# Kernel optimization log

Hardware: AMD Instinct MI355X
Metric: run time of the kernel (lower is better)

Reference implementation:

```python
import jax, jax.numpy as jnp
import numpy as np
import math

MID = 48       # mid_channels
HEADS = 4      # num_heads
POS = 16       # mid_channels // 3 (row/col positional channels)


def _unfold(x, p):
    """nn.Unfold with kernel p, padding p//2: (..., H, W) -> (..., p, p, H, W)."""
    H, W = x.shape[-2], x.shape[-1]
    pad = p // 2
    xp = jnp.pad(x, [(0, 0)] * (x.ndim - 2) + [(pad, pad), (pad, pad)])
    return jnp.stack(
        [jnp.stack([xp[..., k:k + H, l:l + W] for l in range(p)], axis=-3)
         for k in range(p)], axis=-4)


def _pe_mlp(idx, w1, b1, g, b, w2, b2):
    """Conv2d(1->16,1x1) -> LayerNorm(16) -> Swish -> Conv2d(16->POS,1x1) on scalar coords."""
    t = idx.reshape(-1, 1)                         # (N,1)
    h = t @ w1.T + b1                              # (N,16)
    mu = jnp.mean(h, -1, keepdims=True)
    var = jnp.var(h, -1, keepdims=True)
    h = (h - mu) * jax.lax.rsqrt(var + 1e-5) * g + b
    h = h * jax.nn.sigmoid(h)                      # Swish
    e = h @ w2.T + b2                              # (N,POS)
    return e.reshape(idx.shape + (e.shape[-1],))   # (V,P,P,POS)


def setup_inputs() -> dict:
    key = jax.random.key(0)
    ks = jax.random.split(key, 32)
    B, Cin, G, H, W, P, Cout = 2, 32, 4, 28, 28, 7, 64

    def n(k, shp, s=0.05):
        return jax.random.normal(k, shp, dtype=jnp.float32) * s

    inp = {"x": jax.random.normal(ks[0], (B, Cin, G, H, W), dtype=jnp.float32)}
    inp["Wq"] = n(ks[1], (MID * HEADS, Cin)); inp["bq"] = n(ks[2], (MID * HEADS,))
    inp["Wk"] = n(ks[3], (MID * HEADS, Cin)); inp["bk"] = n(ks[4], (MID * HEADS,))
    inp["Wv"] = n(ks[5], (MID * HEADS, Cin)); inp["bv"] = n(ks[6], (MID * HEADS,))
    inp["Wout"] = n(ks[7], (Cout, MID * HEADS)); inp["bout"] = n(ks[8], (Cout,))
    inp["row_w1"] = n(ks[9], (16, 1)); inp["row_b1"] = n(ks[10], (16,))
    inp["row_ln_g"] = jnp.ones((16,), jnp.float32); inp["row_ln_b"] = jnp.zeros((16,), jnp.float32)
    inp["row_w2"] = n(ks[11], (POS, 16)); inp["row_b2"] = n(ks[12], (POS,))
    inp["col_w1"] = n(ks[13], (16, 1)); inp["col_b1"] = n(ks[14], (16,))
    inp["col_ln_g"] = jnp.ones((16,), jnp.float32); inp["col_ln_b"] = jnp.zeros((16,), jnp.float32)
    inp["col_w2"] = n(ks[15], (POS, 16)); inp["col_b2"] = n(ks[16], (POS,))
    inp["group_emb"] = n(ks[17], (G, MID - 2 * POS))
    # rotated relative spatial positions, normalized to [-1, 1]
    lin = np.linspace(-1.0, 1.0, P).astype(np.float32)
    r = np.repeat(lin[:, None], P, 1)
    c = np.repeat(lin[None, :], P, 0)
    rows, cols = [], []
    for v in range(G):
        th = v * math.pi / 2.0
        rows.append(math.cos(th) * r - math.sin(th) * c)
        cols.append(math.sin(th) * r + math.cos(th) * c)
    inp["row_indices"] = jnp.asarray(np.stack(rows, 0))
    inp["col_indices"] = jnp.asarray(np.stack(cols, 0))
    # acted relative group positions for cyclic group C4
    ar = np.arange(G)
    gi = (ar[:, None, None] + ar[None, None, :] - ar[None, :, None]) % G
    inp["g_indices"] = jnp.asarray(gi, dtype=jnp.int32)
    return inp


def _forward(x, Wq, bq, Wk, bk, Wv, bv, Wout, bout,
             row_w1, row_b1, row_ln_g, row_ln_b, row_w2, row_b2,
             col_w1, col_b1, col_ln_g, col_ln_b, col_w2, col_b2,
             group_emb, row_indices, col_indices, g_indices):
    B, Cin, G, H, W = x.shape
    P = row_indices.shape[-1]
    sqn = jnp.sqrt(jnp.float32(Cin))

    def proj(Wm, bm):  # 1x1 Conv3d -> (B, MID, HEADS, G, H, W)
        y = jnp.einsum('oi,bigyx->bogyx', Wm, x) + bm[None, :, None, None, None]
        return y.reshape(B, MID, HEADS, G, H, W)

    q = proj(Wq, bq)
    k = proj(Wk, bk)
    v = proj(Wv, bv)
    k_loc = _unfold(k, P)   # (B, MID, HEADS, G, P, P, H, W)
    v_loc = _unfold(v, P)

    content = jnp.einsum('bchgij,bchmklij->bhgijmkl', q, k_loc)
    row_e = _pe_mlp(row_indices, row_w1, row_b1, row_ln_g, row_ln_b, row_w2, row_b2)
    col_e = _pe_mlp(col_indices, col_w1, col_b1, col_ln_g, col_ln_b, col_w2, col_b2)
    row_s = jnp.einsum('bchgij,vklc->bhvgijkl', q[:, :POS], row_e)
    col_s = jnp.einsum('bchgij,vklc->bhvgijkl', q[:, POS:2 * POS], col_e)
    g_e = group_emb[g_indices]                              # (V, G, M, gdim)
    g_s = jnp.einsum('bchgij,vgmc->bhvgijm', q[:, 2 * POS:], g_e)

    # scores: (b, h, v, g, i, j, m, k, l)
    scores = (row_s[:, :, :, :, :, :, None] + col_s[:, :, :, :, :, :, None]
              + g_s[..., None, None] + content[:, :, None]) / sqn

    # mask patch positions that fall outside the image (-inf -> prob 0)
    valid = _unfold(jnp.ones((H, W), jnp.float32), P)       # (P, P, H, W)
    valid = jnp.transpose(valid, (2, 3, 0, 1))[None, None, None, None, :, :, None, :, :]
    scores = jnp.where(valid > 0.5, scores, -jnp.inf)

    shp = scores.shape
    probs = jax.nn.softmax(scores.reshape(shp[:-3] + (-1,)), axis=-1).reshape(shp)

    o = jnp.einsum('bhvgijmkl,bchmklij->bchvij', probs, v_loc)  # (B, MID, HEADS, V, H, W)
    o = o.reshape(B, MID * HEADS, G, H, W)
    return jnp.einsum('oi,bivyx->bovyx', Wout, o) + bout[None, :, None, None, None]


def reference(x, Wq, bq, Wk, bk, Wv, bv, Wout, bout,
              row_w1, row_b1, row_ln_g, row_ln_b, row_w2, row_b2,
              col_w1, col_b1, col_ln_g, col_ln_b, col_w2, col_b2,
              group_emb, row_indices, col_indices, g_indices):
    return _forward(x, Wq, bq, Wk, bk, Wv, bv, Wout, bout,
                    row_w1, row_b1, row_ln_g, row_ln_b, row_w2, row_b2,
                    col_w1, col_b1, col_ln_g, col_ln_b, col_w2, col_b2,
                    group_emb, row_indices, col_indices, g_indices)
```

## Files before the change

### kernel.cpp

```cpp
#include <hip/hip_runtime.h>
#include <math.h>

#define Bb   2
#define CIN  32
#define Gg   4
#define NH   4
#define Hh   28
#define Ww   28
#define HW   784
#define Pp   7
#define PP   49
#define MID  48
#define COUT 64
#define OC   192

#define QF    0
#define KF    602112
#define VF    1204224
#define OOFF  1806336
#define KBH   75264
#define KM    18816
#define VBH   75264
#define VPL   37632

#define KSCALE 0.2550611135387359f

__device__ unsigned g_peT2[Gg * PP * 16];
__device__ unsigned g_geT2[8 * 64];
__device__ float    g_WT2[OC * COUT];
__device__ float    g_WqT[CIN * OC];
__device__ float    g_WkT[CIN * OC];
__device__ float    g_WvT[CIN * OC];

typedef _Float16 h2f __attribute__((ext_vector_type(2)));

__device__ __forceinline__ unsigned packh2(float a, float b) {
    auto r = __builtin_amdgcn_cvt_pkrtz(a, b);
    return __builtin_bit_cast(unsigned, r);
}

__device__ __forceinline__ float fdot2(unsigned a, unsigned b, float c) {
    return __builtin_amdgcn_fdot2(__builtin_bit_cast(h2f, a),
                                  __builtin_bit_cast(h2f, b), c, false);
}

__device__ __forceinline__ float exp2_fast(float x) {
    float r;
    asm("v_exp_f32 %0, %1" : "=v"(r) : "v"(x));
    return r;
}

__global__ __launch_bounds__(256) void prep_kernel(
    const float* row_w1, const float* row_b1,
    const float* row_g,  const float* row_bb,
    const float* row_w2, const float* row_b2,
    const float* col_w1, const float* col_b1,
    const float* col_g,  const float* col_bb,
    const float* col_w2, const float* col_b2,
    const float* row_idx, const float* col_idx,
    const float* group_emb, const int* g_indices,
    const float* Wout,
    const float* __restrict__ Wq, const float* __restrict__ Wk,
    const float* __restrict__ Wv)
{
    __shared__ float wtmp[16 * 193];
    int tid = threadIdx.x;
    if (blockIdx.x == 1) {
        for (int idx = tid; idx < OC * CIN; idx += 256) {
            int oo = idx >> 5, ci = idx & 31;
            int tp = ci * OC + oo;
            g_WqT[tp] = Wq[idx];
            g_WkT[tp] = Wk[idx];
            g_WvT[tp] = Wv[idx];
        }
        return;
    }
    for (int t = tid; t < 2 * Gg * PP; t += 256) {
        int half = t / (Gg * PP);
        int n    = t - half * (Gg * PP);
        int v = n / PP, kl = n % PP;
        const float* w1 = half ? col_w1 : row_w1;
        const float* b1 = half ? col_b1 : row_b1;
        const float* lg = half ? col_g  : row_g;
        const float* lb = half ? col_bb : row_bb;
        const float* w2 = half ? col_w2 : row_w2;
        const float* b2 = half ? col_b2 : row_b2;
        float tv = half ? col_idx[n] : row_idx[n];

        float hb[16];
        float mean = 0.f;
        for (int k = 0; k < 16; k++) { hb[k] = tv * w1[k] + b1[k]; mean += hb[k]; }
        mean *= (1.f / 16.f);
        float var = 0.f;
        for (int k = 0; k < 16; k++) { float d = hb[k] - mean; var += d * d; }
        var *= (1.f / 16.f);
        float inv = 1.f / sqrtf(var + 1e-5f);
        for (int k = 0; k < 16; k++) {
            float hn = (hb[k] - mean) * inv * lg[k] + lb[k];
            hb[k] = hn / (1.f + expf(-hn));
        }
        float accv[16];
        for (int p = 0; p < 16; p++) {
            float acc = b2[p];
            for (int k = 0; k < 16; k++) acc += hb[k] * w2[p * 16 + k];
            accv[p] = acc * KSCALE;
        }
        for (int i2 = 0; i2 < 8; i2++)
            g_peT2[(v * PP + kl) * 16 + half * 8 + i2] =
                packh2(accv[2 * i2], accv[2 * i2 + 1]);
    }
    for (int t = tid; t < 64; t += 256) {
        int gi = g_indices[t];
        for (int i2 = 0; i2 < 8; i2++)
            g_geT2[i2 * 64 + t] = packh2(group_emb[gi * 16 + 2 * i2] * KSCALE,
                                         group_emb[gi * 16 + 2 * i2 + 1] * KSCALE);
    }
    for (int chunk = 0; chunk < 4; chunk++) {
        int obase = chunk * 16;
        __syncthreads();
        for (int idx = tid; idx < 16 * OC; idx += 256) {
            int ol = idx / OC, t = idx % OC;
            wtmp[ol * 193 + t] = Wout[(obase + ol) * OC + t];
        }
        __syncthreads();
        for (int idx = tid; idx < 16 * OC; idx += 256) {
            int tp = idx / 16, ol = idx % 16;
            int h = tp / MID, c = tp % MID;
            g_WT2[tp * 64 + obase + ol] = wtmp[ol * 193 + c * NH + h];
        }
    }
}

__global__ __launch_bounds__(192) void qkvpe_kernel(const float* __restrict__ x,
    const float* __restrict__ bq, const float* __restrict__ bk,
    const float* __restrict__ bv, float* __restrict__ ws)
{
    __shared__ float xs[2 * CIN * 8];
    int tid = threadIdx.x;
    unsigned* uw = (unsigned*)ws;

    int r = blockIdx.x;
    int jq = r & 3; r >>= 2;
    int i = r % Hh; r /= Hh;
    int gp = r & 1; int b = r >> 1;
    int j0 = jq * 7;

    for (int idx = tid; idx < 2 * CIN * 7; idx += 192) {
        int gs = idx / (CIN * 7), rem = idx % (CIN * 7);
        int ci = rem / 7, jj = rem % 7;
        xs[gs * CIN * 8 + ci * 8 + jj] =
            x[((b * CIN + ci) * Gg + 2 * gp + gs) * HW + i * Ww + j0 + jj];
    }
    __syncthreads();

    int c = tid >> 2, h = tid & 3;
    int bh = b * NH + h;
    int ij0 = i * Ww + j0;
    const float* xs0 = &xs[0];
    const float* xs1 = &xs[CIN * 8];

    #pragma unroll 1
    for (int p = 0; p < 3; p++) {
        const float* WT = (p == 0) ? g_WqT : (p == 1) ? g_WkT : g_WvT;
        const float* bm = (p == 0) ? bq   : (p == 1) ? bk    : bv;
        float bias = bm[tid];
        float w[32];
        #pragma unroll
        for (int ci = 0; ci < 32; ci++) w[ci] = WT[ci * OC + tid];
        float a0[7], a1[7];
        #pragma unroll
        for (int jj = 0; jj < 7; jj++) { a0[jj] = bias; a1[jj] = bias; }
        #pragma unroll
        for (int ci = 0; ci < 32; ci++) {
            float wv = w[ci];
            float4 xA0 = *(const float4*)&xs0[ci * 8];
            float4 xB0 = *(const float4*)&xs0[ci * 8 + 4];
            float4 xA1 = *(const float4*)&xs1[ci * 8];
            float4 xB1 = *(const float4*)&xs1[ci * 8 + 4];
            a0[0] += wv * xA0.x; a0[1] += wv * xA0.y; a0[2] += wv * xA0.z;
            a0[3] += wv * xA0.w; a0[4] += wv * xB0.x; a0[5] += wv * xB0.y;
            a0[6] += wv * xB0.z;
            a1[0] += wv * xA1.x; a1[1] += wv * xA1.y; a1[2] += wv * xA1.z;
            a1[3] += wv * xA1.w; a1[4] += wv * xB1.x; a1[5] += wv * xB1.y;
            a1[6] += wv * xB1.z;
        }
        if (p < 2) {
            float scl = p ? KSCALE : 1.0f;
            int base0 = p ? KF : QF;
            int ob0 = base0 + ((bh * Gg + 2 * gp + 0) * HW + ij0) * 24 + (c >> 1);
            int ob1 = base0 + ((bh * Gg + 2 * gp + 1) * HW + ij0) * 24 + (c >> 1);
            #pragma unroll
            for (int jj = 0; jj < 7; jj++) {
                float v0 = a0[jj] * scl, v1 = a1[jj] * scl;
                float p0 = __shfl_xor(v0, 4, 64);
                float p1 = __shfl_xor(v1, 4, 64);
                if (!((tid >> 2) & 1)) {
                    uw[ob0 + jj * 24] = packh2(v0, p0);
                    uw[ob1 + jj * 24] = packh2(v1, p1);
                }
            }
        } else {
            int vb = VF + ((bh * 2 + gp) * HW + ij0) * 48 + c;
            #pragma unroll
            for (int jj = 0; jj < 7; jj++)
                uw[vb + jj * 48] = packh2(a0[jj], a1[jj]);
        }
    }
}

__global__ __launch_bounds__(256, 4) void attn_kernel(float* __restrict__ ws)
{
    __shared__ __align__(16) unsigned kvb[7000];
    __shared__ __align__(16) unsigned pp2[4][PP][8];
    __shared__ __align__(16) unsigned qp[4][4][32];
    __shared__ __align__(16) float gsm[4][64];

    const int tid  = threadIdx.x;
    const int wave = tid >> 6;
    const int lane = tid & 63;

    int blk = blockIdx.x;
    int j0 = (blk % 7) * 4;
    int i  = (blk / 7) % Hh;
    int bh = blk / (7 * Hh);
    int b = bh >> 2, h = bh & 3;
    int j  = j0 + wave;
    int ij = i * Ww + j;

    const unsigned* uw = (const unsigned*)ws;
    const unsigned* Kf = uw + KF + bh * KBH;
    const unsigned* Vf = uw + VF + bh * VBH;
    float* Ot = ws + OOFF;

    if (lane < 48) {
        int g = lane / 12, c4 = lane % 12;
        uint2 qv = *(const uint2*)&uw[QF + ((bh * Gg + g) * HW + ij) * 24 + c4 * 2];
        qp[wave][g][c4 * 2]     = qv.x;
        qp[wave][g][c4 * 2 + 1] = qv.y;
    }

    #pragma unroll
    for (int s = 0; s < 2; s++) {
        int t = tid + s * 256;
        if (t < 420) {
            int c8 = t % 6, cl = t / 6;
            int gy = i - 3 + cl / 10, gx = j0 - 3 + cl % 10;
            gy = min(max(gy, 0), Hh - 1); gx = min(max(gx, 0), Ww - 1);
            const unsigned* kp = &Kf[(gy * Ww + gx) * 24 + c8 * 4];
            #pragma unroll
            for (int m = 0; m < 4; m++) {
                uint4 kv = *(const uint4*)(kp + m * KM);
                int o = (m * 70 + cl) * 25 + c8 * 4;
                *(uint2*)&kvb[o]     = make_uint2(kv.x, kv.y);
                *(uint2*)&kvb[o + 2] = make_uint2(kv.z, kv.w);
            }
        }
    }

    int kk = lane / Pp, ll = lane % Pp;
    int cell = (lane < PP) ? kk * 10 + ll + wave : 0;
    bool vmask = (lane < PP) && ((unsigned)(i + kk - 3) < Hh) && ((unsigned)(j + ll - 3) < Ww);
    int lclamp = lane < PP ? lane : 0;

    float per[4][4] = {};
    #pragma unroll
    for (int u4 = 0; u4 < 4; u4++) {
        uint4 qA = *(const uint4*)&qp[wave][0][u4 * 4];
        uint4 qB = *(const uint4*)&qp[wave][1][u4 * 4];
        uint4 qC = *(const uint4*)&qp[wave][2][u4 * 4];
        uint4 qD = *(const uint4*)&qp[wave][3][u4 * 4];
        #pragma unroll
        for (int v = 0; v < 4; v++) {
            uint4 pk = *(const uint4*)&g_peT2[(v * PP + lclamp) * 16 + u4 * 4];
            per[v][0] = fdot2(pk.w, qA.w, fdot2(pk.z, qA.z, fdot2(pk.y, qA.y, fdot2(pk.x, qA.x, per[v][0]))));
            per[v][1] = fdot2(pk.w, qB.w, fdot2(pk.z, qB.z, fdot2(pk.y, qB.y, fdot2(pk.x, qB.x, per[v][1]))));
            per[v][2] = fdot2(pk.w, qC.w, fdot2(pk.z, qC.z, fdot2(pk.y, qC.y, fdot2(pk.x, qC.x, per[v][2]))));
            per[v][3] = fdot2(pk.w, qD.w, fdot2(pk.z, qD.z, fdot2(pk.y, qD.y, fdot2(pk.x, qD.x, per[v][3]))));
        }
    }
    if (!vmask) {
        #pragma unroll
        for (int v = 0; v < 4; v++)
            #pragma unroll
            for (int g = 0; g < 4; g++) per[v][g] = -INFINITY;
    }

    {
        int g = (lane >> 2) & 3;
        float ga = 0.f;
        #pragma unroll
        for (int u = 0; u < 8; u++)
            ga = fdot2(g_geT2[u * 64 + lane], qp[wave][g][16 + u], ga);
        gsm[wave][lane] = ga;
    }
    __syncthreads();

    float acc[4][4] = {};
    #pragma unroll 2
    for (int u4 = 0; u4 < 6; u4++) {
        uint4 qA = *(const uint4*)&qp[wave][0][u4 * 4];
        uint4 qB = *(const uint4*)&qp[wave][1][u4 * 4];
        uint4 qC = *(const uint4*)&qp[wave][2][u4 * 4];
        uint4 qD = *(const uint4*)&qp[wave][3][u4 * 4];
        #pragma unroll
        for (int m = 0; m < 4; m++) {
            int base = (m * 70 + cell) * 25 + u4 * 4;
            uint2 k01 = *(const uint2*)&kvb[base];
            uint2 k23 = *(const uint2*)&kvb[base + 2];
            acc[m][0] = fdot2(k23.y, qA.w, fdot2(k23.x, qA.z, fdot2(k01.y, qA.y, fdot2(k01.x, qA.x, acc[m][0]))));
            acc[m][1] = fdot2(k23.y, qB.w, fdot2(k23.x, qB.z, fdot2(k01.y, qB.y, fdot2(k01.x, qB.x, acc[m][1]))));
            acc[m][2] = fdot2(k23.y, qC.w, fdot2(k23.x, qC.z, fdot2(k01.y, qC.y, fdot2(k01.x, qC.x, acc[m][2]))));
            acc[m][3] = fdot2(k23.y, qD.w, fdot2(k23.x, qD.z, fdot2(k01.y, qD.y, fdot2(k01.x, qD.x, acc[m][3]))));
        }
    }

    float ppr[4][4] = {};
    #pragma unroll
    for (int v = 0; v < 4; v++) {
        #pragma unroll
        for (int g = 0; g < 4; g++) {
            int vg = v * 4 + g;
            float4 gs = *(const float4*)&gsm[wave][vg * 4];
            float ex[4];
            ex[0] = exp2_fast(acc[0][g] + per[v][g] + gs.x);
            ex[1] = exp2_fast(acc[1][g] + per[v][g] + gs.y);
            ex[2] = exp2_fast(acc[2][g] + per[v][g] + gs.z);
            ex[3] = exp2_fast(acc[3][g] + per[v][g] + gs.w);
            float ls = ex[0] + ex[1] + ex[2] + ex[3];
            #pragma unroll
            for (int d = 32; d > 0; d >>= 1) ls += __shfl_xor(ls, d, 64);
            float rinv = 1.0f / ls;
            #pragma unroll
            for (int m = 0; m < 4; m++) ppr[v][m] += ex[m] * rinv;
        }
    }
    if (lane < PP) {
        uint4 w0, w1;
        w0.x = packh2(ppr[0][0], ppr[0][1]); w0.y = packh2(ppr[0][2], ppr[0][3]);
        w0.z = packh2(ppr[1][0], ppr[1][1]); w0.w = packh2(ppr[1][2], ppr[1][3]);
        w1.x = packh2(ppr[2][0], ppr[2][1]); w1.y = packh2(ppr[2][2], ppr[2][3]);
        w1.z = packh2(ppr[3][0], ppr[3][1]); w1.w = packh2(ppr[3][2], ppr[3][3]);
        *(uint4*)&pp2[wave][lane][0] = w0;
        *(uint4*)&pp2[wave][lane][4] = w1;
    }
    __syncthreads();

    for (int t = tid; t < 840; t += 256) {
        int c4 = t % 12, cl = t / 12;
        int gy = i - 3 + cl / 10, gx = j0 - 3 + cl % 10;
        gy = min(max(gy, 0), Hh - 1); gx = min(max(gx, 0), Ww - 1);
        int off = (gy * Ww + gx) * 48 + c4 * 4;
        uint4 A = *(const uint4*)&Vf[off];
        uint4 B = *(const uint4*)&Vf[VPL + off];
        int o = cl * 48 + c4 * 4;
        *(uint4*)&kvb[o]        = A;
        *(uint4*)&kvb[3360 + o] = B;
    }
    __syncthreads();

    if (lane < MID) {
        float o0 = 0.f, o1 = 0.f, o2 = 0.f, o3 = 0.f;
        const uint4* ppw = (const uint4*)&pp2[wave][0][0];
        const unsigned* v0b = &kvb[wave * 48 + lane];
        const unsigned* v1b = v0b + 3360;
        #pragma unroll
        for (int kl2 = 0; kl2 < PP; kl2++) {
            int cellc = (kl2 / Pp) * 10 + (kl2 % Pp);
            unsigned vv0 = v0b[cellc * 48];
            unsigned vv1 = v1b[cellc * 48];
            uint4 A = ppw[kl2 * 2];
            uint4 B = ppw[kl2 * 2 + 1];
            o0 = fdot2(vv1, A.y, fdot2(vv0, A.x, o0));
            o1 = fdot2(vv1, A.w, fdot2(vv0, A.z, o1));
            o2 = fdot2(vv1, B.y, fdot2(vv0, B.x, o2));
            o3 = fdot2(vv1, B.w, fdot2(vv0, B.z, o3));
        }
        Ot[((size_t)(b * Gg + 0) * HW + ij) * OC + h * MID + lane] = o0;
        Ot[((size_t)(b * Gg + 1) * HW + ij) * OC + h * MID + lane] = o1;
        Ot[((size_t)(b * Gg + 2) * HW + ij) * OC + h * MID + lane] = o2;
        Ot[((size_t)(b * Gg + 3) * HW + ij) * OC + h * MID + lane] = o3;
    }
}

__global__ __launch_bounds__(256) void outproj_kernel(const float* __restrict__ bout,
                                                      const float* __restrict__ ws,
                                                      float* __restrict__ out)
{
    __shared__ float ov[16 * 193];
    __shared__ float res[64 * 17];
    int tid = threadIdx.x;
    int p0 = blockIdx.x * 16;
    const float* Ot = ws + OOFF;

    for (int idx = tid; idx < 16 * OC; idx += 256) {
        int pl = idx / OC, t = idx % OC;
        ov[pl * 193 + t] = Ot[(size_t)(p0 + pl) * OC + t];
    }
    __syncthreads();

    int o = tid & 63, pg = tid >> 6;
    float a0 = bout[o], a1 = a0, a2 = a0, a3 = a0;
    #pragma unroll 8
    for (int t = 0; t < OC; t++) {
        float w = g_WT2[t * 64 + o];
        a0 += w * ov[(pg     ) * 193 + t];
        a1 += w * ov[(pg +  4) * 193 + t];
        a2 += w * ov[(pg +  8) * 193 + t];
        a3 += w * ov[(pg + 12) * 193 + t];
    }
    res[o * 17 + pg     ] = a0;
    res[o * 17 + pg +  4] = a1;
    res[o * 17 + pg +  8] = a2;
    res[o * 17 + pg + 12] = a3;
    __syncthreads();

    for (int idx = tid; idx < 1024; idx += 256) {
        int o2 = idx >> 4, pl = idx & 15;
        int p = p0 + pl;
        int ij2 = p % HW; int bv = p / HW; int v = bv & 3; int bb = bv >> 2;
        out[((bb * COUT + o2) * Gg + v) * HW + ij2] = res[o2 * 17 + pl];
    }
}

extern "C" void kernel_launch(void* const* d_in, const int* in_sizes, int n_in,
                              void* d_out, int out_size, void* d_ws, size_t ws_size,
                              hipStream_t stream)
{
    const float* x      = (const float*)d_in[0];
    const float* Wq     = (const float*)d_in[1];
    const float* bq     = (const float*)d_in[2];
    const float* Wk     = (const float*)d_in[3];
    const float* bk     = (const float*)d_in[4];
    const float* Wv     = (const float*)d_in[5];
    const float* bv     = (const float*)d_in[6];
    const float* Wout   = (const float*)d_in[7];
    const float* bout   = (const float*)d_in[8];
    const float* row_w1 = (const float*)d_in[9];
    const float* row_b1 = (const float*)d_in[10];
    const float* row_g  = (const float*)d_in[11];
    const float* row_bb = (const float*)d_in[12];
    const float* row_w2 = (const float*)d_in[13];
    const float* row_b2 = (const float*)d_in[14];
    const float* col_w1 = (const float*)d_in[15];
    const float* col_b1 = (const float*)d_in[16];
    const float* col_g  = (const float*)d_in[17];
    const float* col_bb = (const float*)d_in[18];
    const float* col_w2 = (const float*)d_in[19];
    const float* col_b2 = (const float*)d_in[20];
    const float* gemb   = (const float*)d_in[21];
    const float* ridx   = (const float*)d_in[22];
    const float* cidx   = (const float*)d_in[23];
    const int*   gidx   = (const int*)d_in[24];

    float* ws  = (float*)d_ws;
    float* out = (float*)d_out;

    prep_kernel<<<2, 256, 0, stream>>>(
        row_w1, row_b1, row_g, row_bb, row_w2, row_b2,
        col_w1, col_b1, col_g, col_bb, col_w2, col_b2,
        ridx, cidx, gemb, gidx, Wout, Wq, Wk, Wv);
    qkvpe_kernel<<<Bb * 2 * Hh * 4, 192, 0, stream>>>(x, bq, bk, bv, ws);
    attn_kernel<<<Bb * NH * Hh * (Ww / 4), 256, 0, stream>>>(ws);
    outproj_kernel<<<Bb * Gg * HW / 16, 256, 0, stream>>>(bout, ws, out);
}
```

Measured before the change: 207.6 us.

## Move PE/Wout prep into QKV kernel and widen QKV tiles to 14 columns

```diff
diff --git a/kernel.cpp b/kernel.cpp
--- a/kernel.cpp
+++ b/kernel.cpp
@@ -51,6 +51,24 @@
 }
 
 __global__ __launch_bounds__(256) void prep_kernel(
+    const float* __restrict__ Wq, const float* __restrict__ Wk,
+    const float* __restrict__ Wv)
+{
+    int tid = threadIdx.x;
+    for (int idx = tid; idx < CIN * OC; idx += 256) {
+        int t = idx % OC;
+        int ci = idx / OC;
+        int oo = (t % MID) * NH + t / MID;
+        int src = oo * CIN + ci;
+        g_WqT[idx] = Wq[src];
+        g_WkT[idx] = Wk[src];
+        g_WvT[idx] = Wv[src];
+    }
+}
+
+__global__ __launch_bounds__(192) void qkvpe_kernel(const float* __restrict__ x,
+    const float* __restrict__ bq, const float* __restrict__ bk,
+    const float* __restrict__ bv,
     const float* row_w1, const float* row_b1,
     const float* row_g,  const float* row_bb,
     const float* row_w2, const float* row_b2,
@@ -60,152 +78,146 @@
     const float* row_idx, const float* col_idx,
     const float* group_emb, const int* g_indices,
     const float* Wout,
-    const float* __restrict__ Wq, const float* __restrict__ Wk,
-    const float* __restrict__ Wv)
+    float* __restrict__ ws)
 {
+    __shared__ float xs[2 * CIN * 16];
     __shared__ float wtmp[16 * 193];
     int tid = threadIdx.x;
-    if (blockIdx.x == 1) {
-        for (int idx = tid; idx < OC * CIN; idx += 256) {
-            int oo = idx >> 5, ci = idx & 31;
-            int tp = ci * OC + oo;
-            g_WqT[tp] = Wq[idx];
-            g_WkT[tp] = Wk[idx];
-            g_WvT[tp] = Wv[idx];
+    unsigned* uw = (unsigned*)ws;
+    if (blockIdx.x == Bb * 2 * Hh * 2) {
+        for (int t = tid; t < 2 * Gg * PP; t += 192) {
+            int half = t / (Gg * PP);
+            int n    = t - half * (Gg * PP);
+            int v = n / PP, kl = n % PP;
+            const float* w1 = half ? col_w1 : row_w1;
+            const float* b1 = half ? col_b1 : row_b1;
+            const float* lg = half ? col_g  : row_g;
+            const float* lb = half ? col_bb : row_bb;
+            const float* w2 = half ? col_w2 : row_w2;
+            const float* b2 = half ? col_b2 : row_b2;
+            float tv = half ? col_idx[n] : row_idx[n];
+
+            float hb[16];
+            float mean = 0.f;
+            for (int k = 0; k < 16; k++) { hb[k] = tv * w1[k] + b1[k]; mean += hb[k]; }
+            mean *= (1.f / 16.f);
+            float var = 0.f;
+            for (int k = 0; k < 16; k++) { float d = hb[k] - mean; var += d * d; }
+            var *= (1.f / 16.f);
+            float inv = 1.f / sqrtf(var + 1e-5f);
+            for (int k = 0; k < 16; k++) {
+                float hn = (hb[k] - mean) * inv * lg[k] + lb[k];
+                hb[k] = hn / (1.f + expf(-hn));
+            }
+            float accv[16];
+            for (int p = 0; p < 16; p++) {
+                float acc = b2[p];
+                for (int k = 0; k < 16; k++) acc += hb[k] * w2[p * 16 + k];
+                accv[p] = acc * KSCALE;
+            }
+            for (int i2 = 0; i2 < 8; i2++)
+                g_peT2[(v * PP + kl) * 16 + half * 8 + i2] =
+                    packh2(accv[2 * i2], accv[2 * i2 + 1]);
+        }
+        for (int t = tid; t < 64; t += 192) {
+            int gi = g_indices[t];
+            for (int i2 = 0; i2 < 8; i2++)
+                g_geT2[i2 * 64 + t] = packh2(group_emb[gi * 16 + 2 * i2] * KSCALE,
+                                             group_emb[gi * 16 + 2 * i2 + 1] * KSCALE);
+        }
+        for (int chunk = 0; chunk < 4; chunk++) {
+            int obase = chunk * 16;
+            __syncthreads();
+            for (int idx = tid; idx < 16 * OC; idx += 192) {
+                int ol = idx / OC, t = idx % OC;
+                wtmp[ol * 193 + t] = Wout[(obase + ol) * OC + t];
+            }
+            __syncthreads();
+            for (int idx = tid; idx < 16 * OC; idx += 192) {
+                int tp = idx / 16, ol = idx % 16;
+                int h = tp / MID, c = tp % MID;
+                g_WT2[tp * 64 + obase + ol] = wtmp[ol * 193 + c * NH + h];
+            }
         }
         return;
     }
-    for (int t = tid; t < 2 * Gg * PP; t += 256) {
-        int half = t / (Gg * PP);
-        int n    = t - half * (Gg * PP);
-        int v = n / PP, kl = n % PP;
-        const float* w1 = half ? col_w1 : row_w1;
-        const float* b1 = half ? col_b1 : row_b1;
-        const float* lg = half ? col_g  : row_g;
-        const float* lb = half ? col_bb : row_bb;
-        const float* w2 = half ? col_w2 : row_w2;
-        const float* b2 = half ? col_b2 : row_b2;
-        float tv = half ? col_idx[n] : row_idx[n];
-
-        float hb[16];
-        float mean = 0.f;
-        for (int k = 0; k < 16; k++) { hb[k] = tv * w1[k] + b1[k]; mean += hb[k]; }
-        mean *= (1.f / 16.f);
-        float var = 0.f;
-        for (int k = 0; k < 16; k++) { float d = hb[k] - mean; var += d * d; }
-        var *= (1.f / 16.f);
-        float inv = 1.f / sqrtf(var + 1e-5f);
-        for (int k = 0; k < 16; k++) {
-            float hn = (hb[k] - mean) * inv * lg[k] + lb[k];
-            hb[k] = hn / (1.f + expf(-hn));
-        }
-        float accv[16];
-        for (int p = 0; p < 16; p++) {
-            float acc = b2[p];
-            for (int k = 0; k < 16; k++) acc += hb[k] * w2[p * 16 + k];
-            accv[p] = acc * KSCALE;
-        }
-        for (int i2 = 0; i2 < 8; i2++)
-            g_peT2[(v * PP + kl) * 16 + half * 8 + i2] =
-                packh2(accv[2 * i2], accv[2 * i2 + 1]);
-    }
-    for (int t = tid; t < 64; t += 256) {
-        int gi = g_indices[t];
-        for (int i2 = 0; i2 < 8; i2++)
-            g_geT2[i2 * 64 + t] = packh2(group_emb[gi * 16 + 2 * i2] * KSCALE,
-                                         group_emb[gi * 16 + 2 * i2 + 1] * KSCALE);
-    }
-    for (int chunk = 0; chunk < 4; chunk++) {
-        int obase = chunk * 16;
-        __syncthreads();
-        for (int idx = tid; idx < 16 * OC; idx += 256) {
-            int ol = idx / OC, t = idx % OC;
-            wtmp[ol * 193 + t] = Wout[(obase + ol) * OC + t];
-        }
-        __syncthreads();
-        for (int idx = tid; idx < 16 * OC; idx += 256) {
-            int tp = idx / 16, ol = idx % 16;
-            int h = tp / MID, c = tp % MID;
-            g_WT2[tp * 64 + obase + ol] = wtmp[ol * 193 + c * NH + h];
-        }
-    }
-}
-
-__global__ __launch_bounds__(192) void qkvpe_kernel(const float* __restrict__ x,
-    const float* __restrict__ bq, const float* __restrict__ bk,
-    const float* __restrict__ bv, float* __restrict__ ws)
-{
-    __shared__ float xs[2 * CIN * 8];
-    int tid = threadIdx.x;
-    unsigned* uw = (unsigned*)ws;
 
     int r = blockIdx.x;
-    int jq = r & 3; r >>= 2;
+    int jh = r & 1; r >>= 1;
     int i = r % Hh; r /= Hh;
     int gp = r & 1; int b = r >> 1;
-    int j0 = jq * 7;
-
-    for (int idx = tid; idx < 2 * CIN * 7; idx += 192) {
-        int gs = idx / (CIN * 7), rem = idx % (CIN * 7);
-        int ci = rem / 7, jj = rem % 7;
-        xs[gs * CIN * 8 + ci * 8 + jj] =
+    int j0 = jh * 14;
+
+    for (int idx = tid; idx < 2 * CIN * 14; idx += 192) {
+        int gs = idx / (CIN * 14), rem = idx % (CIN * 14);
+        int ci = rem / 14, jj = rem % 14;
+        xs[gs * CIN * 16 + ci * 16 + jj] =
             x[((b * CIN + ci) * Gg + 2 * gp + gs) * HW + i * Ww + j0 + jj];
     }
     __syncthreads();
 
-    int c = tid >> 2, h = tid & 3;
+    int h = tid / MID, c = tid % MID;
+    int oo = c * NH + h;
     int bh = b * NH + h;
     int ij0 = i * Ww + j0;
     const float* xs0 = &xs[0];
-    const float* xs1 = &xs[CIN * 8];
+    const float* xs1 = &xs[CIN * 16];
+
+#define CONV14R(A, XR)                                                        \
+    {                                                                         \
+        _Pragma("unroll")                                                     \
+        for (int jj = 0; jj < 14; jj++) A[jj] = bias;                         \
+        _Pragma("unroll")                                                     \
+        for (int ci = 0; ci < 32; ci++) {                                     \
+            float wv = w[ci];                                                 \
+            float4 xA = *(const float4*)&XR[ci * 16 + 0];                     \
+            float4 xB = *(const float4*)&XR[ci * 16 + 4];                     \
+            float4 xC = *(const float4*)&XR[ci * 16 + 8];                     \
+            float2 xD = *(const float2*)&XR[ci * 16 + 12];                    \
+            A[0] += wv * xA.x;  A[1] += wv * xA.y;  A[2] += wv * xA.z;        \
+            A[3] += wv * xA.w;  A[4] += wv * xB.x;  A[5] += wv * xB.y;        \
+            A[6] += wv * xB.z;  A[7] += wv * xB.w;  A[8] += wv * xC.x;        \
+            A[9] += wv * xC.y;  A[10] += wv * xC.z; A[11] += wv * xC.w;       \
+            A[12] += wv * xD.x; A[13] += wv * xD.y;                           \
+        }                                                                     \
+    }
 
     #pragma unroll 1
-    for (int p = 0; p < 3; p++) {
-        const float* WT = (p == 0) ? g_WqT : (p == 1) ? g_WkT : g_WvT;
-        const float* bm = (p == 0) ? bq   : (p == 1) ? bk    : bv;
-        float bias = bm[tid];
+    for (int p = 0; p < 2; p++) {
+        const float* WT = p ? g_WkT : g_WqT;
+        float bias = (p ? bk : bq)[oo];
+        float scl  = p ? KSCALE : 1.0f;
+        int base0  = p ? KF : QF;
         float w[32];
         #pragma unroll
         for (int ci = 0; ci < 32; ci++) w[ci] = WT[ci * OC + tid];
-        float a0[7], a1[7];
-        #pragma unroll
-        for (int jj = 0; jj < 7; jj++) { a0[jj] = bias; a1[jj] = bias; }
-        #pragma unroll
-        for (int ci = 0; ci < 32; ci++) {
-            float wv = w[ci];
-            float4 xA0 = *(const float4*)&xs0[ci * 8];
-            float4 xB0 = *(const float4*)&xs0[ci * 8 + 4];
-            float4 xA1 = *(const float4*)&xs1[ci * 8];
-            float4 xB1 = *(const float4*)&xs1[ci * 8 + 4];
-            a0[0] += wv * xA0.x; a0[1] += wv * xA0.y; a0[2] += wv * xA0.z;
-            a0[3] += wv * xA0.w; a0[4] += wv * xB0.x; a0[5] += wv * xB0.y;
-            a0[6] += wv * xB0.z;
-            a1[0] += wv * xA1.x; a1[1] += wv * xA1.y; a1[2] += wv * xA1.z;
-            a1[3] += wv * xA1.w; a1[4] += wv * xB1.x; a1[5] += wv * xB1.y;
-            a1[6] += wv * xB1.z;
-        }
-        if (p < 2) {
-            float scl = p ? KSCALE : 1.0f;
-            int base0 = p ? KF : QF;
-            int ob0 = base0 + ((bh * Gg + 2 * gp + 0) * HW + ij0) * 24 + (c >> 1);
-            int ob1 = base0 + ((bh * Gg + 2 * gp + 1) * HW + ij0) * 24 + (c >> 1);
+        #pragma unroll 1
+        for (int gs = 0; gs < 2; gs++) {
+            float a[14];
+            CONV14R(a, (gs ? xs1 : xs0))
+            int ob = base0 + ((bh * Gg + 2 * gp + gs) * HW + ij0) * 24 + (c >> 1);
             #pragma unroll
-            for (int jj = 0; jj < 7; jj++) {
-                float v0 = a0[jj] * scl, v1 = a1[jj] * scl;
-                float p0 = __shfl_xor(v0, 4, 64);
-                float p1 = __shfl_xor(v1, 4, 64);
-                if (!((tid >> 2) & 1)) {
-                    uw[ob0 + jj * 24] = packh2(v0, p0);
-                    uw[ob1 + jj * 24] = packh2(v1, p1);
-                }
-            }
-        } else {
-            int vb = VF + ((bh * 2 + gp) * HW + ij0) * 48 + c;
-            #pragma unroll
-            for (int jj = 0; jj < 7; jj++)
-                uw[vb + jj * 48] = packh2(a0[jj], a1[jj]);
-        }
-    }
+            for (int jj = 0; jj < 14; jj++) {
+                float av = a[jj] * scl;
+                float pr = __shfl_xor(av, 1, 64);
+                if (!(tid & 1)) uw[ob + jj * 24] = packh2(av, pr);
+            }
+        }
+    }
+    {
+        float bias = bv[oo];
+        float w[32];
+        #pragma unroll
+        for (int ci = 0; ci < 32; ci++) w[ci] = g_WvT[ci * OC + tid];
+        float a0[14], a1[14];
+        CONV14R(a0, xs0)
+        CONV14R(a1, xs1)
+        int vb = VF + ((bh * 2 + gp) * HW + ij0) * 48 + c;
+        #pragma unroll
+        for (int jj = 0; jj < 14; jj++)
+            uw[vb + jj * 48] = packh2(a0[jj], a1[jj]);
+    }
+#undef CONV14R
 }
 
 __global__ __launch_bounds__(256, 4) void attn_kernel(float* __restrict__ ws)
@@ -455,11 +467,12 @@
     float* ws  = (float*)d_ws;
     float* out = (float*)d_out;
 
-    prep_kernel<<<2, 256, 0, stream>>>(
+    prep_kernel<<<1, 256, 0, stream>>>(Wq, Wk, Wv);
+    qkvpe_kernel<<<Bb * 2 * Hh * 2 + 1, 192, 0, stream>>>(
+        x, bq, bk, bv,
         row_w1, row_b1, row_g, row_bb, row_w2, row_b2,
         col_w1, col_b1, col_g, col_bb, col_w2, col_b2,
-        ridx, cidx, gemb, gidx, Wout, Wq, Wk, Wv);
-    qkvpe_kernel<<<Bb * 2 * Hh * 4, 192, 0, stream>>>(x, bq, bk, bv, ws);
+        ridx, cidx, gemb, gidx, Wout, ws);
     attn_kernel<<<Bb * NH * Hh * (Ww / 4), 256, 0, stream>>>(ws);
     outproj_kernel<<<Bb * Gg * HW / 16, 256, 0, stream>>>(bout, ws, out);
 }
```

After: 442.1 us. +113.0%, slower.
